# Kernel optimization log

Hardware: AMD Instinct MI355X
Metric: run time of the kernel (lower is better)

The kernel has to match this reference:

```python
import jax, jax.numpy as jnp
import numpy as np

D_MODEL = 1024
N_HEADS = 16
D_HEAD = D_MODEL // N_HEADS


def setup_inputs() -> dict:
    key = jax.random.key(0)
    ks = jax.random.split(key, 16)
    B, S, D = 2, 2048, D_MODEL
    s = 1.0 / np.sqrt(D)
    inp = {
        "query": jax.random.normal(ks[0], (B, S, D), jnp.float32),
        "key": jax.random.normal(ks[1], (B, S, D), jnp.float32),
        "value": jax.random.normal(ks[2], (B, S, D), jnp.float32),
        "pos_embedding": jax.random.normal(ks[3], (B, S, D), jnp.float32),
        "Wq": jax.random.normal(ks[4], (D, D), jnp.float32) * s,
        "bq": jnp.zeros((D,), jnp.float32),
        "Wk": jax.random.normal(ks[5], (D, D), jnp.float32) * s,
        "bk": jnp.zeros((D,), jnp.float32),
        "Wv": jax.random.normal(ks[6], (D, D), jnp.float32) * s,
        "bv": jnp.zeros((D,), jnp.float32),
        "Wpos": jax.random.normal(ks[7], (D, D), jnp.float32) * s,
        "u_bias": jax.random.normal(ks[8], (N_HEADS, D_HEAD), jnp.float32) * s,
        "v_bias": jax.random.normal(ks[9], (N_HEADS, D_HEAD), jnp.float32) * s,
        "Wout": jax.random.normal(ks[10], (D, D), jnp.float32) * s,
        "bout": jnp.zeros((D,), jnp.float32),
    }
    return inp


def _rel_shift(pos_score):
    # Transformer-XL relative shift: pad one zero column, reshape, drop first row.
    B, H, S1, S2 = pos_score.shape
    zeros = jnp.zeros((B, H, S1, 1), pos_score.dtype)
    padded = jnp.concatenate([zeros, pos_score], axis=-1)  # [B,H,S1,S2+1]
    padded = padded.reshape(B, H, S2 + 1, S1)
    return padded[:, :, 1:].reshape(B, H, S1, S2)


def reference(query, key, value, pos_embedding, Wq, bq, Wk, bk, Wv, bv, Wpos, u_bias, v_bias, Wout, bout):
    B, S, D = query.shape
    H, dh = N_HEADS, D_HEAD
    q = (query @ Wq + bq).reshape(B, S, H, dh)            # [B,S,H,dh]
    k = (key @ Wk + bk).reshape(B, S, H, dh)              # [B,S,H,dh]
    v = (value @ Wv + bv).reshape(B, S, H, dh)            # [B,S,H,dh]
    p = (pos_embedding @ Wpos).reshape(B, S, H, dh)       # [B,S,H,dh]

    content_score = jnp.einsum('bqhd,bkhd->bhqk', q + u_bias, k)
    pos_score = jnp.einsum('bqhd,bkhd->bhqk', q + v_bias, p)
    pos_score = _rel_shift(pos_score)

    score = (content_score + pos_score) / jnp.asarray(np.sqrt(D), score_dtype := content_score.dtype)
    attn = jax.nn.softmax(score, axis=-1)                 # [B,H,S,S]
    context = jnp.einsum('bhqk,bkhd->bqhd', attn, v).reshape(B, S, D)
    out = context @ Wout + bout
    return out, attn
```

## Files before the change

### kernel.cpp

```cpp
#include <hip/hip_runtime.h>

#define S_LEN 2048
#define DM    1024
#define NH    16
#define DH    64
#define BATCH 2
#define S2    ((size_t)S_LEN * S_LEN)
#define CTXSZ ((size_t)BATCH * S_LEN * DM)

typedef _Float16 half_t;
typedef _Float16 f16x8 __attribute__((ext_vector_type(8)));
typedef float    f32x4 __attribute__((ext_vector_type(4)));

__device__ __forceinline__ void gll16(const void* g, void* l) {
  __builtin_amdgcn_global_load_lds(
      (const __attribute__((address_space(1))) void*)g,
      (__attribute__((address_space(3))) void*)l, 16, 0, 0);
}

__device__ __forceinline__ void stage_gll(half_t* lds, const half_t* src, int stride) {
  const int t = threadIdx.x, w = t >> 6, lane = t & 63;
  const int c1 = lane & 7, r8 = lane >> 3;
#pragma unroll
  for (int it = 0; it < 4; ++it) {
    int r = w * 32 + it * 8 + r8;
    const half_t* g = src + (size_t)r * stride + ((c1 ^ r8) << 3);
    gll16(g, lds + (size_t)w * 2048 + it * 512);
  }
}

__device__ __forceinline__ void mfma_block(const half_t* At, const half_t* Bt,
                                           int w, int lane, f32x4 acc[2][8]) {
  const int grp = lane >> 4, li = lane & 15;
#pragma unroll
  for (int ks = 0; ks < 2; ++ks) {
    const int chunk = ks * 4 + grp;
    f16x8 a[2], b[8];
#pragma unroll
    for (int fr = 0; fr < 2; ++fr) {
      int r = w * 32 + fr * 16 + li;
      a[fr] = *(const f16x8*)&At[(size_t)(r * 8 + (chunk ^ (r & 7))) * 8];
    }
#pragma unroll
    for (int fc = 0; fc < 8; ++fc) {
      int r = fc * 16 + li;
      b[fc] = *(const f16x8*)&Bt[(size_t)(r * 8 + (chunk ^ (r & 7))) * 8];
    }
#pragma unroll
    for (int fr = 0; fr < 2; ++fr)
#pragma unroll
      for (int fc = 0; fc < 8; ++fc)
        acc[fr][fc] = __builtin_amdgcn_mfma_f32_16x16x32_f16(a[fr], b[fc], acc[fr][fc], 0, 0, 0);
  }
}

template<typename ST>
__device__ __forceinline__ void load8s(const ST* p, float* o) {
  if constexpr (sizeof(ST) == 2) {
    f16x8 v = *(const f16x8*)p;
#pragma unroll
    for (int e = 0; e < 8; ++e) o[e] = (float)v[e];
  } else {
    const float4* q = (const float4*)p;
    float4 a = q[0], b = q[1];
    o[0]=a.x; o[1]=a.y; o[2]=a.z; o[3]=a.w; o[4]=b.x; o[5]=b.y; o[6]=b.z; o[7]=b.w;
  }
}

struct PArgs {
  const float* asrc[4]; half_t* adst[4];
  const float* wsrc[5]; half_t* wdst[5];
};

__global__ __launch_bounds__(256) void prep(PArgs pa, half_t* zbuf) {
  __shared__ float T[64][65];
  const int bx = blockIdx.x, t = threadIdx.x;
  if (bx < 8192) {
    if (bx == 0 && t < 8) {
      float4 z = {0.f, 0.f, 0.f, 0.f};
      ((float4*)zbuf)[t] = z;
    }
    const int mat = bx >> 11, blk = bx & 2047;
    const float* s = pa.asrc[mat];
    half_t* d = pa.adst[mat];
    size_t i = ((size_t)blk * 256 + t) * 8;
    float4 v0 = *(const float4*)(s + i), v1 = *(const float4*)(s + i + 4);
    f16x8 h;
    h[0]=(half_t)v0.x; h[1]=(half_t)v0.y; h[2]=(half_t)v0.z; h[3]=(half_t)v0.w;
    h[4]=(half_t)v1.x; h[5]=(half_t)v1.y; h[6]=(half_t)v1.z; h[7]=(half_t)v1.w;
    *(f16x8*)(d + i) = h;
  } else {
    const int idx = bx - 8192;
    const int z = idx >> 8, rem = idx & 255;
    const int k0 = (rem & 15) * 64, n0 = (rem >> 4) * 64;
    const float* W = pa.wsrc[z];
    half_t* D = pa.wdst[z];
#pragma unroll
    for (int it = 0; it < 4; ++it) {
      int id2 = t + it * 256; int r = id2 >> 4, c4 = (id2 & 15) * 4;
      float4 v = *(const float4*)(W + (size_t)(k0 + r) * DM + n0 + c4);
      T[r][c4] = v.x; T[r][c4 + 1] = v.y; T[r][c4 + 2] = v.z; T[r][c4 + 3] = v.w;
    }
    __syncthreads();
#pragma unroll
    for (int it = 0; it < 2; ++it) {
      int id2 = t + it * 256; int n = id2 >> 3, kc = (id2 & 7) * 8;
      f16x8 o;
#pragma unroll
      for (int e = 0; e < 8; ++e) o[e] = (half_t)T[kc + e][n];
      *(f16x8*)&D[(size_t)(n0 + n) * DM + k0 + kc] = o;
    }
  }
}

struct GArgs {
  const half_t* A[4];  const half_t* Bt[4];
  const float* ba[4]; const float* bu[4]; const float* bv[4];
  half_t* oa[4]; half_t* ob[4]; float* of[4];
};

template<bool F32OUT>
__global__ __launch_bounds__(256) void gemm_k(GArgs g, int K) {
  __shared__ __align__(16) half_t At[128 * 64];
  __shared__ __align__(16) half_t Bt[128 * 64];
  const int lin = blockIdx.x + 8 * (blockIdx.y + 32 * blockIdx.z);
  const int nwg = 8 * 32 * gridDim.z;
  const int xcd = lin & 7, tt = lin >> 3;
  const int grpid = xcd * (nwg >> 6) + (tt >> 3);
  const int n0 = (tt & 7) * 128;
  const int z = grpid >> 5;
  const int m0 = (grpid & 31) * 128;

  const half_t* A = g.A[z];
  const half_t* B = g.Bt[z];
  const int t = threadIdx.x, w = t >> 6, lane = t & 63;
  const f32x4 zf = {0.f, 0.f, 0.f, 0.f};
  f32x4 acc[2][8];
#pragma unroll
  for (int i = 0; i < 2; ++i)
#pragma unroll
    for (int j = 0; j < 8; ++j) acc[i][j] = zf;

  for (int k0 = 0; k0 < K; k0 += 64) {
    stage_gll(At, A + (size_t)m0 * K + k0, K);
    stage_gll(Bt, B + (size_t)n0 * K + k0, K);
    __syncthreads();
    mfma_block(At, Bt, w, lane, acc);
    __syncthreads();
  }
  const int grp = lane >> 4, li = lane & 15;
#pragma unroll
  for (int fr = 0; fr < 2; ++fr)
#pragma unroll
    for (int fc = 0; fc < 8; ++fc)
#pragma unroll
      for (int r = 0; r < 4; ++r) {
        int row = m0 + w * 32 + fr * 16 + grp * 4 + r;
        int col = n0 + fc * 16 + li;
        float v = acc[fr][fc][r];
        if (g.ba[z]) v += g.ba[z][col];
        if constexpr (F32OUT) {
          g.of[z][(size_t)row * DM + col] = v;
        } else {
          float v1 = v + (g.bu[z] ? g.bu[z][col] : 0.f);
          g.oa[z][(size_t)row * DM + col] = (half_t)v1;
          if (g.ob[z]) g.ob[z][(size_t)row * DM + col] = (half_t)(v + g.bv[z][col]);
        }
      }
}

__global__ __launch_bounds__(256) void vtrans(const half_t* vp, half_t* vT) {
  __shared__ half_t T[64][72];
  const int s0 = blockIdx.x * 64, h = blockIdx.y, b = blockIdx.z;
  const int t = threadIdx.x;
#pragma unroll
  for (int it = 0; it < 2; ++it) {
    int idx = t + it * 256; int s = idx >> 3, c = idx & 7;
    uint4 v = *(const uint4*)(vp + ((size_t)(b * S_LEN + s0 + s)) * DM + h * DH + c * 8);
    *(uint4*)&T[s][c * 8] = v;
  }
  __syncthreads();
  half_t* dst = vT + ((size_t)(b * NH + h)) * DH * S_LEN;
#pragma unroll
  for (int it = 0; it < 2; ++it) {
    int idx = t + it * 256; int d = idx >> 3, sc = (idx & 7) * 8;
    f16x8 o;
#pragma unroll
    for (int e = 0; e < 8; ++e) o[e] = T[sc + e][d];
    *(f16x8*)&dst[(size_t)d * S_LEN + s0 + sc] = o;
  }
}

template<typename ST>
__global__ __launch_bounds__(512, 6) void score_fused(
    const half_t* __restrict__ qu_, const half_t* __restrict__ qv_,
    const half_t* __restrict__ kp_, const half_t* __restrict__ pp_,
    const half_t* __restrict__ zbuf, ST* __restrict__ sc, float* __restrict__ part)
{
  __shared__ __align__(16) half_t MsR[16896];
  __shared__ __align__(16) half_t QV[128 * 64];
  half_t* QU = MsR;
  half_t* Kt = MsR + 8192;
  half_t* Ms = MsR;

  const int bh = blockIdx.z, b = bh >> 4, h = bh & 15;
  const int kt = blockIdx.x, qt = blockIdx.y;
  const int i0 = qt * 128, k0 = kt * 128;
  const int base = 1920 + k0 - i0;
  const int t = threadIdx.x, w = t >> 6, lane = t & 63;
  const int grp = lane >> 4, li = lane & 15;

  {
    const half_t* srcA = qu_ + ((size_t)(b * S_LEN + i0)) * DM + h * DH;
    const half_t* srcB = kp_ + ((size_t)(b * S_LEN + k0)) * DM + h * DH;
    const half_t* srcQ = qv_ + ((size_t)(b * S_LEN + i0)) * DM + h * DH;
#pragma unroll
    for (int p = 0; p < 2; ++p) {
      int cidx = t + p * 512; int r = cidx >> 3, c = cidx & 7;
      size_t off = (size_t)r * DM + ((c ^ (r & 7)) << 3);
      gll16(srcA + off, QU + (size_t)cidx * 8);
      gll16(srcB + off, Kt + (size_t)cidx * 8);
      gll16(srcQ + off, QV + (size_t)cidx * 8);
    }
  }

  const int e0 = w * 16 + li, e1 = (w + 8) * 16 + li;
  const int dlt0 = (base + e0 >= S_LEN + 1) ? 1 : 0;
  const int dlt1 = (base + e1 >= S_LEN + 1) ? 1 : 0;
  f16x8 bm[2][2];
#pragma unroll
  for (int eci = 0; eci < 2; ++eci) {
    int e_row = eci ? e1 : e0;
    int jv = base + e_row; if (jv >= S_LEN + 1) jv -= (S_LEN + 1);
    const half_t* srcp = (jv == S_LEN) ? zbuf
        : pp_ + ((size_t)(b * S_LEN + jv)) * DM + h * DH;
#pragma unroll
    for (int kk = 0; kk < 2; ++kk)
      bm[kk][eci] = *(const f16x8*)(srcp + (kk * 4 + grp) * 8);
  }
  __syncthreads();

  const f32x4 zf = {0.f, 0.f, 0.f, 0.f};
  f32x4 acc_c[8];
#pragma unroll
  for (int j = 0; j < 8; ++j) acc_c[j] = zf;
#pragma unroll
  for (int kk = 0; kk < 2; ++kk) {
    const int chunk = kk * 4 + grp;
    int ra = w * 16 + li;
    f16x8 a = *(const f16x8*)&QU[(size_t)(ra * 8 + (chunk ^ (ra & 7))) * 8];
#pragma unroll
    for (int fc = 0; fc < 8; ++fc) {
      int rb = fc * 16 + li;
      f16x8 bf = *(const f16x8*)&Kt[(size_t)(rb * 8 + (chunk ^ (rb & 7))) * 8];
      acc_c[fc] = __builtin_amdgcn_mfma_f32_16x16x32_f16(a, bf, acc_c[fc], 0, 0, 0);
    }
  }
  __syncthreads();

  const int C0 = e0 - 127 - 133 * dlt0;
  const int C1 = e1 - 127 - 133 * dlt1;
  int lo0 = 127 + dlt0 - e0; if (lo0 < dlt0) lo0 = dlt0;
  int hi0 = 254 + dlt0 - e0; if (hi0 > 127) hi0 = 127;
  int lo1 = 127 + dlt1 - e1; if (lo1 < dlt1) lo1 = dlt1;
  int hi1 = 254 + dlt1 - e1; if (hi1 > 127) hi1 = 127;

  for (int rf = 0; rf < 8; ++rf) {
    f32x4 am[2] = {zf, zf};
#pragma unroll
    for (int kk = 0; kk < 2; ++kk) {
      int ra = rf * 16 + li;
      f16x8 a = *(const f16x8*)&QV[(size_t)(ra * 8 + ((kk * 4 + grp) ^ (ra & 7))) * 8];
      am[0] = __builtin_amdgcn_mfma_f32_16x16x32_f16(a, bm[kk][0], am[0], 0, 0, 0);
      am[1] = __builtin_amdgcn_mfma_f32_16x16x32_f16(a, bm[kk][1], am[1], 0, 0, 0);
    }
    const int rMb = rf * 16 + grp * 4;
    {
      int addr = rMb * 133 + C0;
#pragma unroll
      for (int r = 0; r < 4; ++r) {
        int rM = rMb + r;
        if (rM >= lo0 && rM <= hi0) Ms[addr + 133 * r] = (half_t)am[0][r];
      }
    }
    {
      int addr = rMb * 133 + C1;
#pragma unroll
      for (int r = 0; r < 4; ++r) {
        int rM = rMb + r;
        if (rM >= lo1 && rM <= hi1) Ms[addr + 133 * r] = (half_t)am[1][r];
      }
    }
  }

  {
    f16x8 aq0, aq1;
    {
      int r128 = i0 + 128; if (r128 > S_LEN - 1) r128 = S_LEN - 1;
      const half_t* q128p = qv_ + ((size_t)(b * S_LEN + r128)) * DM + h * DH;
      aq0 = *(const f16x8*)(q128p + (0 * 4 + grp) * 8);
      aq1 = *(const f16x8*)(q128p + (1 * 4 + grp) * 8);
    }
    f32x4 am0 = zf;
    am0 = __builtin_amdgcn_mfma_f32_16x16x32_f16(aq0, bm[0][0], am0, 0, 0, 0);
    am0 = __builtin_amdgcn_mfma_f32_16x16x32_f16(aq1, bm[1][0], am0, 0, 0, 0);
    if (grp == 0 && dlt0 == 1)
      Ms[127 * 132 + e0] = (half_t)am0[0];
  }
  __syncthreads();

  ST* sb = sc + (size_t)bh * S2;
  const int qb = w * 16 + grp * 4;
  const half_t* MsB = Ms + qb * 132 + li;
  ST* sbB = sb + (size_t)(i0 + qb) * S_LEN + k0 + li;
  float lsum[4];
#pragma unroll
  for (int rr = 0; rr < 4; ++rr) {
    const half_t* mrow = MsB + rr * 132;
    ST* srow = sbB + (size_t)rr * S_LEN;
    float acc = 0.f;
#pragma unroll
    for (int fc = 0; fc < 8; ++fc) {
      float mval = (float)mrow[fc * 16];
      float s = (acc_c[fc][rr] + mval) * 0.03125f;
      float ev = __expf(s);
      srow[fc * 16] = (ST)ev;
      acc += ev;
    }
    lsum[rr] = acc;
  }
#pragma unroll
  for (int rr = 0; rr < 4; ++rr) {
    float v = lsum[rr];
#pragma unroll
    for (int d = 1; d < 16; d <<= 1) v += __shfl_xor(v, d);
    if (li == 0)
      part[((size_t)bh * S_LEN + i0 + qb + rr) * 16 + kt] = v;
  }
}

template<typename ST>
__global__ __launch_bounds__(256) void av_attn(const ST* sc, const half_t* vT, const float* part,
                                               float* attn, half_t* ctx) {
  __shared__ __align__(16) half_t Vt[2][64 * 128];
  __shared__ float Ls[128];
  const int bh = blockIdx.y, b = bh >> 4, h = bh & 15;
  const int q0 = blockIdx.x * 128;
  const int t = threadIdx.x;
  if (t < 128) {
    const float* pp = part + ((size_t)bh * S_LEN + q0 + t) * 16;
    float L = 0.f;
#pragma unroll
    for (int k = 0; k < 16; ++k) L += pp[k];
    Ls[t] = 1.f / L;
  }
  const ST* sb = sc + (size_t)bh * S2;
  float* ab = attn + (size_t)bh * S2;
  const half_t* vb = vT + (size_t)bh * (DH * S_LEN);
  const int w = t >> 6, lane = t & 63, grp = lane >> 4, li = lane & 15;
  const int c1 = lane & 15, d4 = lane >> 4;
  const f32x4 zf = {0.f, 0.f, 0.f, 0.f};
  f32x4 acc[2][4];
#pragma unroll
  for (int i = 0; i < 2; ++i)
#pragma unroll
    for (int j = 0; j < 4; ++j) acc[i][j] = zf;

#pragma unroll
  for (int it = 0; it < 4; ++it) {
    int d = w * 16 + it * 4 + d4;
    gll16(vb + (size_t)d * S_LEN + ((c1 ^ (d & 15)) << 3), Vt[0] + (size_t)w * 2048 + it * 512);
  }
  __syncthreads();
  int cur = 0;

  for (int kt = 0; kt < 16; ++kt) {
    if (kt + 1 < 16) {
#pragma unroll
      for (int it = 0; it < 4; ++it) {
        int d = w * 16 + it * 4 + d4;
        gll16(vb + (size_t)d * S_LEN + (kt + 1) * 128 + ((c1 ^ (d & 15)) << 3),
              Vt[cur ^ 1] + (size_t)w * 2048 + it * 512);
      }
    }
#pragma unroll
    for (int ks = 0; ks < 4; ++ks) {
      f16x8 pa[2];
#pragma unroll
      for (int fr = 0; fr < 2; ++fr) {
        int r128 = w * 32 + fr * 16 + li;
        int row = q0 + r128;
        int col = kt * 128 + ks * 32 + grp * 8;
        float sv[8];
        load8s(&sb[(size_t)row * S_LEN + col], sv);
        float rL = Ls[r128];
#pragma unroll
        for (int e = 0; e < 8; ++e) sv[e] *= rL;
        float4* dst = (float4*)&ab[(size_t)row * S_LEN + col];
        float4 w0 = {sv[0], sv[1], sv[2], sv[3]};
        float4 w1 = {sv[4], sv[5], sv[6], sv[7]};
        dst[0] = w0; dst[1] = w1;
        f16x8 ph;
#pragma unroll
        for (int e = 0; e < 8; ++e) ph[e] = (half_t)sv[e];
        pa[fr] = ph;
      }
      f16x8 bf[4];
#pragma unroll
      for (int fc = 0; fc < 4; ++fc) {
        int d = fc * 16 + li; int chunk = ks * 4 + grp;
        bf[fc] = *(const f16x8*)&Vt[cur][(size_t)(d * 16 + (chunk ^ (d & 15))) * 8];
      }
#pragma unroll
      for (int fr = 0; fr < 2; ++fr)
#pragma unroll
        for (int fc = 0; fc < 4; ++fc)
          acc[fr][fc] = __builtin_amdgcn_mfma_f32_16x16x32_f16(pa[fr], bf[fc], acc[fr][fc], 0, 0, 0);
    }
    __syncthreads();
    cur ^= 1;
  }
#pragma unroll
  for (int fr = 0; fr < 2; ++fr)
#pragma unroll
    for (int fc = 0; fc < 4; ++fc)
#pragma unroll
      for (int r = 0; r < 4; ++r) {
        int q = q0 + w * 32 + fr * 16 + grp * 4 + r;
        int d = fc * 16 + li;
        ctx[((size_t)(b * S_LEN + q)) * DM + h * DH + d] = (half_t)acc[fr][fc][r];
      }
}

extern "C" void kernel_launch(void* const* d_in, const int* in_sizes, int n_in,
                              void* d_out, int out_size, void* d_ws, size_t ws_size,
                              hipStream_t stream) {
  (void)in_sizes; (void)n_in; (void)out_size;

  const float* query  = (const float*)d_in[0];
  const float* key    = (const float*)d_in[1];
  const float* value  = (const float*)d_in[2];
  const float* pos    = (const float*)d_in[3];
  const float* Wq     = (const float*)d_in[4];
  const float* bq     = (const float*)d_in[5];
  const float* Wk     = (const float*)d_in[6];
  const float* bk     = (const float*)d_in[7];
  const float* Wv     = (const float*)d_in[8];
  const float* bv     = (const float*)d_in[9];
  const float* Wpos   = (const float*)d_in[10];
  const float* u_bias = (const float*)d_in[11];
  const float* v_bias = (const float*)d_in[12];
  const float* Wout   = (const float*)d_in[13];
  const float* bout   = (const float*)d_in[14];

  float* out  = (float*)d_out;
  float* attn = out + (size_t)BATCH * S_LEN * DM;

  char* ws = (char*)d_ws;
  half_t* Wt   = (half_t*)(ws);
  half_t* Af16 = (half_t*)(ws + 10485760);
  float*  part = (float*)(ws + 10485760);
  half_t* qu   = (half_t*)(ws + 44040192);
  half_t* qv   = (half_t*)(ws + 52428800);
  half_t* kp   = (half_t*)(ws + 60817408);
  half_t* pp   = (half_t*)(ws + 69206016);
  half_t* vp   = (half_t*)(ws + 77594624);
  half_t* vT   = (half_t*)(ws + 85983232);
  half_t* ctx  = (half_t*)(ws + 77594624);
  half_t* zbuf = (half_t*)(ws + 94371840);
  half_t* scH  = (half_t*)(ws + 94375936);
  const bool fast = ws_size >= (size_t)94375936 + (size_t)BATCH * NH * S2 * 2;

  dim3 blk(256);

  PArgs pa;
  pa.asrc[0] = query; pa.asrc[1] = key; pa.asrc[2] = value; pa.asrc[3] = pos;
  for (int i = 0; i < 4; ++i) pa.adst[i] = Af16 + (size_t)i * CTXSZ;
  pa.wsrc[0] = Wq; pa.wsrc[1] = Wk; pa.wsrc[2] = Wv; pa.wsrc[3] = Wpos; pa.wsrc[4] = Wout;
  for (int i = 0; i < 5; ++i) pa.wdst[i] = Wt + (size_t)i * DM * DM;
  prep<<<dim3(8192 + 1280), blk, 0, stream>>>(pa, zbuf);

  GArgs ga{};
  for (int i = 0; i < 4; ++i) {
    ga.A[i]  = Af16 + (size_t)i * CTXSZ;
    ga.Bt[i] = Wt + (size_t)i * DM * DM;
  }
  ga.ba[0] = bq; ga.ba[1] = bk; ga.ba[2] = bv; ga.ba[3] = nullptr;
  ga.bu[0] = u_bias; ga.bv[0] = v_bias;
  ga.oa[0] = qu; ga.oa[1] = kp; ga.oa[2] = vp; ga.oa[3] = pp;
  ga.ob[0] = qv;
  gemm_k<false><<<dim3(8, 32, 4), blk, 0, stream>>>(ga, DM);

  vtrans<<<dim3(32, 16, 2), blk, 0, stream>>>(vp, vT);

  dim3 g_sc(16, 16, 32);
  dim3 blk5(512);
  if (fast) {
    score_fused<half_t><<<g_sc, blk5, 0, stream>>>(qu, qv, kp, pp, zbuf, scH, part);
    av_attn<half_t><<<dim3(16, 32), blk, 0, stream>>>(scH, vT, part, attn, ctx);
  } else {
    float* scF = attn;
    score_fused<float><<<g_sc, blk5, 0, stream>>>(qu, qv, kp, pp, zbuf, scF, part);
    av_attn<float><<<dim3(16, 32), blk, 0, stream>>>(scF, vT, part, attn, ctx);
  }

  GArgs go{};
  go.A[0] = ctx; go.Bt[0] = Wt + (size_t)4 * DM * DM;
  go.ba[0] = bout; go.of[0] = out;
  gemm_k<true><<<dim3(8, 32, 1), blk, 0, stream>>>(go, DM);
}
```

Measured before the change: 513.9 us.

## Split score/AV into per-batch chunks, widen AV blocks, use nontemporal attn stores

The score and attention-times-V kernels now run in two launches of 16 batch-heads each, interleaved. The intent is that the fp16 score buffer written by one chunk is still in L2/LLC when the AV kernel reads it. The AV kernel moves to 512 threads with 16 rows per wave, halving per-thread accumulators and V staging. The fp32 attn output is written with nontemporal stores so it does not evict the cached scores. Costs are extra launches, less parallelism per launch and more waves sharing LDS.

```diff
diff --git a/kernel.cpp b/kernel.cpp
--- a/kernel.cpp
+++ b/kernel.cpp
@@ -195,7 +195,8 @@
 __global__ __launch_bounds__(512, 6) void score_fused(
     const half_t* __restrict__ qu_, const half_t* __restrict__ qv_,
     const half_t* __restrict__ kp_, const half_t* __restrict__ pp_,
-    const half_t* __restrict__ zbuf, ST* __restrict__ sc, float* __restrict__ part)
+    const half_t* __restrict__ zbuf, ST* __restrict__ sc, float* __restrict__ part,
+    int bh0)
 {
   __shared__ __align__(16) half_t MsR[16896];
   __shared__ __align__(16) half_t QV[128 * 64];
@@ -203,7 +204,7 @@
   half_t* Kt = MsR + 8192;
   half_t* Ms = MsR;
 
-  const int bh = blockIdx.z, b = bh >> 4, h = bh & 15;
+  const int bh = bh0 + blockIdx.z, b = bh >> 4, h = bh & 15;
   const int kt = blockIdx.x, qt = blockIdx.y;
   const int i0 = qt * 128, k0 = kt * 128;
   const int base = 1920 + k0 - i0;
@@ -340,11 +341,11 @@
 }
 
 template<typename ST>
-__global__ __launch_bounds__(256) void av_attn(const ST* sc, const half_t* vT, const float* part,
-                                               float* attn, half_t* ctx) {
+__global__ __launch_bounds__(512) void av_attn(const ST* sc, const half_t* vT, const float* part,
+                                               float* attn, half_t* ctx, int bh0) {
   __shared__ __align__(16) half_t Vt[2][64 * 128];
   __shared__ float Ls[128];
-  const int bh = blockIdx.y, b = bh >> 4, h = bh & 15;
+  const int bh = bh0 + blockIdx.y, b = bh >> 4, h = bh & 15;
   const int q0 = blockIdx.x * 128;
   const int t = threadIdx.x;
   if (t < 128) {
@@ -360,16 +361,15 @@
   const int w = t >> 6, lane = t & 63, grp = lane >> 4, li = lane & 15;
   const int c1 = lane & 15, d4 = lane >> 4;
   const f32x4 zf = {0.f, 0.f, 0.f, 0.f};
-  f32x4 acc[2][4];
-#pragma unroll
-  for (int i = 0; i < 2; ++i)
-#pragma unroll
-    for (int j = 0; j < 4; ++j) acc[i][j] = zf;
-
-#pragma unroll
-  for (int it = 0; it < 4; ++it) {
-    int d = w * 16 + it * 4 + d4;
-    gll16(vb + (size_t)d * S_LEN + ((c1 ^ (d & 15)) << 3), Vt[0] + (size_t)w * 2048 + it * 512);
+  f32x4 acc[4];
+#pragma unroll
+  for (int j = 0; j < 4; ++j) acc[j] = zf;
+
+#pragma unroll
+  for (int it = 0; it < 2; ++it) {
+    int d = w * 8 + it * 4 + d4;
+    gll16(vb + (size_t)d * S_LEN + ((c1 ^ (d & 15)) << 3),
+          Vt[0] + (size_t)(w * 2 + it) * 512);
   }
   __syncthreads();
   int cur = 0;
@@ -377,34 +377,30 @@
   for (int kt = 0; kt < 16; ++kt) {
     if (kt + 1 < 16) {
 #pragma unroll
-      for (int it = 0; it < 4; ++it) {
-        int d = w * 16 + it * 4 + d4;
+      for (int it = 0; it < 2; ++it) {
+        int d = w * 8 + it * 4 + d4;
         gll16(vb + (size_t)d * S_LEN + (kt + 1) * 128 + ((c1 ^ (d & 15)) << 3),
-              Vt[cur ^ 1] + (size_t)w * 2048 + it * 512);
+              Vt[cur ^ 1] + (size_t)(w * 2 + it) * 512);
       }
     }
 #pragma unroll
     for (int ks = 0; ks < 4; ++ks) {
-      f16x8 pa[2];
-#pragma unroll
-      for (int fr = 0; fr < 2; ++fr) {
-        int r128 = w * 32 + fr * 16 + li;
-        int row = q0 + r128;
-        int col = kt * 128 + ks * 32 + grp * 8;
-        float sv[8];
-        load8s(&sb[(size_t)row * S_LEN + col], sv);
-        float rL = Ls[r128];
-#pragma unroll
-        for (int e = 0; e < 8; ++e) sv[e] *= rL;
-        float4* dst = (float4*)&ab[(size_t)row * S_LEN + col];
-        float4 w0 = {sv[0], sv[1], sv[2], sv[3]};
-        float4 w1 = {sv[4], sv[5], sv[6], sv[7]};
-        dst[0] = w0; dst[1] = w1;
-        f16x8 ph;
-#pragma unroll
-        for (int e = 0; e < 8; ++e) ph[e] = (half_t)sv[e];
-        pa[fr] = ph;
-      }
+      const int r128 = w * 16 + li;
+      const int row = q0 + r128;
+      const int col = kt * 128 + ks * 32 + grp * 8;
+      float sv[8];
+      load8s(&sb[(size_t)row * S_LEN + col], sv);
+      float rL = Ls[r128];
+#pragma unroll
+      for (int e = 0; e < 8; ++e) sv[e] *= rL;
+      f32x4* dst = (f32x4*)&ab[(size_t)row * S_LEN + col];
+      f32x4 w0 = {sv[0], sv[1], sv[2], sv[3]};
+      f32x4 w1 = {sv[4], sv[5], sv[6], sv[7]};
+      __builtin_nontemporal_store(w0, dst);
+      __builtin_nontemporal_store(w1, dst + 1);
+      f16x8 pa;
+#pragma unroll
+      for (int e = 0; e < 8; ++e) pa[e] = (half_t)sv[e];
       f16x8 bf[4];
 #pragma unroll
       for (int fc = 0; fc < 4; ++fc) {
@@ -412,24 +408,20 @@
         bf[fc] = *(const f16x8*)&Vt[cur][(size_t)(d * 16 + (chunk ^ (d & 15))) * 8];
       }
 #pragma unroll
-      for (int fr = 0; fr < 2; ++fr)
-#pragma unroll
-        for (int fc = 0; fc < 4; ++fc)
-          acc[fr][fc] = __builtin_amdgcn_mfma_f32_16x16x32_f16(pa[fr], bf[fc], acc[fr][fc], 0, 0, 0);
+      for (int fc = 0; fc < 4; ++fc)
+        acc[fc] = __builtin_amdgcn_mfma_f32_16x16x32_f16(pa, bf[fc], acc[fc], 0, 0, 0);
     }
     __syncthreads();
     cur ^= 1;
   }
 #pragma unroll
-  for (int fr = 0; fr < 2; ++fr)
-#pragma unroll
-    for (int fc = 0; fc < 4; ++fc)
-#pragma unroll
-      for (int r = 0; r < 4; ++r) {
-        int q = q0 + w * 32 + fr * 16 + grp * 4 + r;
-        int d = fc * 16 + li;
-        ctx[((size_t)(b * S_LEN + q)) * DM + h * DH + d] = (half_t)acc[fr][fc][r];
-      }
+  for (int fc = 0; fc < 4; ++fc)
+#pragma unroll
+    for (int r = 0; r < 4; ++r) {
+      int q = q0 + w * 16 + grp * 4 + r;
+      int d = fc * 16 + li;
+      ctx[((size_t)(b * S_LEN + q)) * DM + h * DH + d] = (half_t)acc[fc][r];
+    }
 }
 
 extern "C" void kernel_launch(void* const* d_in, const int* in_sizes, int n_in,
@@ -493,15 +485,22 @@
 
   vtrans<<<dim3(32, 16, 2), blk, 0, stream>>>(vp, vT);
 
-  dim3 g_sc(16, 16, 32);
   dim3 blk5(512);
   if (fast) {
-    score_fused<half_t><<<g_sc, blk5, 0, stream>>>(qu, qv, kp, pp, zbuf, scH, part);
-    av_attn<half_t><<<dim3(16, 32), blk, 0, stream>>>(scH, vT, part, attn, ctx);
+    for (int g = 0; g < 2; ++g) {
+      score_fused<half_t><<<dim3(16, 16, 16), blk5, 0, stream>>>(
+          qu, qv, kp, pp, zbuf, scH, part, g * 16);
+      av_attn<half_t><<<dim3(16, 16), blk5, 0, stream>>>(
+          scH, vT, part, attn, ctx, g * 16);
+    }
   } else {
     float* scF = attn;
-    score_fused<float><<<g_sc, blk5, 0, stream>>>(qu, qv, kp, pp, zbuf, scF, part);
-    av_attn<float><<<dim3(16, 32), blk, 0, stream>>>(scF, vT, part, attn, ctx);
+    for (int g = 0; g < 2; ++g) {
+      score_fused<float><<<dim3(16, 16, 16), blk5, 0, stream>>>(
+          qu, qv, kp, pp, zbuf, scF, part, g * 16);
+      av_attn<float><<<dim3(16, 16), blk5, 0, stream>>>(
+          scF, vT, part, attn, ctx, g * 16);
+    }
   }
 
   GArgs go{};
```

New measurement: 537.5 us. 4.6% more time.

## Split normalized attn write out of PV kernel into a streaming scale kernel

Applied to the files above, without the earlier changes.

The PV kernel no longer writes the normalized fp32 attention matrix. It feeds the raw exponentiated scores straight into the MFMAs and applies the 1/L row normalization to the context in its epilogue. A new per-row attn_scale kernel with one block per row reads the scores, scales them and writes attn. The aim is to move the large attention write from a 512-block kernel into a highly parallel streaming kernel. The cost is a second full read of the score buffer and an extra launch.

```diff
diff --git a/kernel.cpp b/kernel.cpp
--- a/kernel.cpp
+++ b/kernel.cpp
@@ -51,19 +51,6 @@
 #pragma unroll
       for (int fc = 0; fc < 8; ++fc)
         acc[fr][fc] = __builtin_amdgcn_mfma_f32_16x16x32_f16(a[fr], b[fc], acc[fr][fc], 0, 0, 0);
-  }
-}
-
-template<typename ST>
-__device__ __forceinline__ void load8s(const ST* p, float* o) {
-  if constexpr (sizeof(ST) == 2) {
-    f16x8 v = *(const f16x8*)p;
-#pragma unroll
-    for (int e = 0; e < 8; ++e) o[e] = (float)v[e];
-  } else {
-    const float4* q = (const float4*)p;
-    float4 a = q[0], b = q[1];
-    o[0]=a.x; o[1]=a.y; o[2]=a.z; o[3]=a.w; o[4]=b.x; o[5]=b.y; o[6]=b.z; o[7]=b.w;
   }
 }
 
@@ -340,8 +327,8 @@
 }
 
 template<typename ST>
-__global__ __launch_bounds__(256) void av_attn(const ST* sc, const half_t* vT, const float* part,
-                                               float* attn, half_t* ctx) {
+__global__ __launch_bounds__(256) void av_pv(const ST* sc, const half_t* vT, const float* part,
+                                             half_t* ctx) {
   __shared__ __align__(16) half_t Vt[2][64 * 128];
   __shared__ float Ls[128];
   const int bh = blockIdx.y, b = bh >> 4, h = bh & 15;
@@ -355,7 +342,6 @@
     Ls[t] = 1.f / L;
   }
   const ST* sb = sc + (size_t)bh * S2;
-  float* ab = attn + (size_t)bh * S2;
   const half_t* vb = vT + (size_t)bh * (DH * S_LEN);
   const int w = t >> 6, lane = t & 63, grp = lane >> 4, li = lane & 15;
   const int c1 = lane & 15, d4 = lane >> 4;
@@ -385,25 +371,21 @@
     }
 #pragma unroll
     for (int ks = 0; ks < 4; ++ks) {
+      const int col = kt * 128 + ks * 32 + grp * 8;
       f16x8 pa[2];
 #pragma unroll
       for (int fr = 0; fr < 2; ++fr) {
-        int r128 = w * 32 + fr * 16 + li;
-        int row = q0 + r128;
-        int col = kt * 128 + ks * 32 + grp * 8;
-        float sv[8];
-        load8s(&sb[(size_t)row * S_LEN + col], sv);
-        float rL = Ls[r128];
-#pragma unroll
-        for (int e = 0; e < 8; ++e) sv[e] *= rL;
-        float4* dst = (float4*)&ab[(size_t)row * S_LEN + col];
-        float4 w0 = {sv[0], sv[1], sv[2], sv[3]};
-        float4 w1 = {sv[4], sv[5], sv[6], sv[7]};
-        dst[0] = w0; dst[1] = w1;
-        f16x8 ph;
-#pragma unroll
-        for (int e = 0; e < 8; ++e) ph[e] = (half_t)sv[e];
-        pa[fr] = ph;
+        const int row = q0 + w * 32 + fr * 16 + li;
+        if constexpr (sizeof(ST) == 2) {
+          pa[fr] = *(const f16x8*)&sb[(size_t)row * S_LEN + col];
+        } else {
+          const f32x4* sp = (const f32x4*)&sb[(size_t)row * S_LEN + col];
+          f32x4 a = sp[0], bq = sp[1];
+          f16x8 ph;
+#pragma unroll
+          for (int e = 0; e < 4; ++e) { ph[e] = (half_t)a[e]; ph[4 + e] = (half_t)bq[e]; }
+          pa[fr] = ph;
+        }
       }
       f16x8 bf[4];
 #pragma unroll
@@ -426,10 +408,38 @@
     for (int fc = 0; fc < 4; ++fc)
 #pragma unroll
       for (int r = 0; r < 4; ++r) {
-        int q = q0 + w * 32 + fr * 16 + grp * 4 + r;
+        int rq = w * 32 + fr * 16 + grp * 4 + r;
+        int q = q0 + rq;
         int d = fc * 16 + li;
-        ctx[((size_t)(b * S_LEN + q)) * DM + h * DH + d] = (half_t)acc[fr][fc][r];
-      }
+        ctx[((size_t)(b * S_LEN + q)) * DM + h * DH + d] = (half_t)(acc[fr][fc][r] * Ls[rq]);
+      }
+}
+
+template<typename ST>
+__global__ __launch_bounds__(256) void attn_scale(const ST* sc, const float* part,
+                                                  float* attn) {
+  const size_t row = blockIdx.x;
+  const float* pp = part + row * 16;
+  float L = 0.f;
+#pragma unroll
+  for (int k = 0; k < 16; ++k) L += pp[k];
+  const float rL = 1.f / L;
+  const int t = threadIdx.x;
+  float* o = attn + row * S_LEN + t * 8;
+  if constexpr (sizeof(ST) == 2) {
+    f16x8 v = *(const f16x8*)(sc + row * S_LEN + t * 8);
+    f32x4 w0, w1;
+#pragma unroll
+    for (int e = 0; e < 4; ++e) { w0[e] = (float)v[e] * rL; w1[e] = (float)v[4 + e] * rL; }
+    ((f32x4*)o)[0] = w0;
+    ((f32x4*)o)[1] = w1;
+  } else {
+    f32x4* op = (f32x4*)o;
+    f32x4 a = op[0], bq = op[1];
+#pragma unroll
+    for (int e = 0; e < 4; ++e) { a[e] *= rL; bq[e] *= rL; }
+    op[0] = a; op[1] = bq;
+  }
 }
 
 extern "C" void kernel_launch(void* const* d_in, const int* in_sizes, int n_in,
@@ -495,13 +505,16 @@
 
   dim3 g_sc(16, 16, 32);
   dim3 blk5(512);
+  const int nrows = BATCH * NH * S_LEN;
   if (fast) {
     score_fused<half_t><<<g_sc, blk5, 0, stream>>>(qu, qv, kp, pp, zbuf, scH, part);
-    av_attn<half_t><<<dim3(16, 32), blk, 0, stream>>>(scH, vT, part, attn, ctx);
+    av_pv<half_t><<<dim3(16, 32), blk, 0, stream>>>(scH, vT, part, ctx);
+    attn_scale<half_t><<<dim3(nrows), blk, 0, stream>>>(scH, part, attn);
   } else {
     float* scF = attn;
     score_fused<float><<<g_sc, blk5, 0, stream>>>(qu, qv, kp, pp, zbuf, scF, part);
-    av_attn<float><<<dim3(16, 32), blk, 0, stream>>>(scF, vT, part, attn, ctx);
+    av_pv<float><<<dim3(16, 32), blk, 0, stream>>>(scF, vT, part, ctx);
+    attn_scale<float><<<dim3(nrows), blk, 0, stream>>>(scF, part, attn);
   }
 
   GArgs go{};
```

Measured after the change: 493.5 us (median of 2 runs). -4.0%, faster.
